# Optimization experiments

Measured on AMD Instinct MI355X. Metric: run time of the kernel, lower is better.

Reference implementation:

```python
import jax, jax.numpy as jnp
import numpy as np

N = 50000      # nodes
E = 800000     # edges (avg degree 16)
IN = 256       # in_feats
H = 128        # hidden_feats
C = 40         # out_feats == num classes (label dim)
LPA_ITERS = 10


def setup_inputs() -> dict:
    key = jax.random.key(0)
    ks = jax.random.split(key, 9)
    features = jax.random.normal(ks[0], (N, IN), dtype=jnp.float32)
    labels = jax.random.normal(ks[1], (N, C), dtype=jnp.float32)
    mask = jax.random.randint(ks[2], (N,), 0, 2) > 0          # bool [N]
    src = jax.random.randint(ks[3], (E,), 0, N, dtype=jnp.int32)
    dst = jax.random.randint(ks[4], (E,), 0, N, dtype=jnp.int32)
    W1 = jax.random.normal(ks[5], (IN, H), dtype=jnp.float32) * (1.0 / np.sqrt(IN))
    b1 = jnp.zeros((H,), dtype=jnp.float32)
    W2 = jax.random.normal(ks[6], (H, C), dtype=jnp.float32) * (1.0 / np.sqrt(H))
    b2 = jnp.zeros((C,), dtype=jnp.float32)
    return {"features": features, "labels": labels, "mask": mask,
            "src": src, "dst": dst, "W1": W1, "b1": b1, "W2": W2, "b2": b2}


def reference(features, labels, mask, src, dst, W1, b1, W2, b2):
    ones_e = jnp.ones((E,), dtype=jnp.float32)
    deg_out = jax.ops.segment_sum(ones_e, src, num_segments=N)  # out-degree
    deg_in = jax.ops.segment_sum(ones_e, dst, num_segments=N)   # in-degree
    norm_src = jnp.maximum(deg_out, 1.0) ** -0.5                 # DGL clamps deg>=1
    norm_dst = jnp.maximum(deg_in, 1.0) ** -0.5

    def gconv(x, W, b):
        # DGL GraphConv, norm='both': D_in^{-1/2} A^T D_out^{-1/2} (x W) + b
        h = (x @ W) * norm_src[:, None]                          # [N, d_out]
        agg = jax.ops.segment_sum(h[src], dst, num_segments=N)   # gather+scatter-add
        return agg * norm_dst[:, None] + b

    x = jax.nn.relu(gconv(features, W1, b1))
    # dropout identity in eval mode
    x = gconv(x, W2, b2)

    # Label propagation: adj[src,dst]=1 so (adj @ y)[i] = sum_{(i->j)} y[j]
    masked_labels = jnp.where(mask[:, None], labels, 0.0)

    def step(y, _):
        y = jax.ops.segment_sum(y[dst], src, num_segments=N)
        y = jnp.where(mask[:, None], labels, y)
        return y, None

    y, _ = jax.lax.scan(step, masked_labels, None, length=LPA_ITERS)
    return x, y
```

## Files before the change

### kernel.cpp

```cpp
#include <hip/hip_runtime.h>

#define Nn 50000
#define Ee 800000
#define INF_ 256
#define HID 128
#define NC 40
#define CAPD 48
#define CAPS 48
#define LPA_ITERS 10
#define NB 98
#define BSH 9
#define EPB 1024
#define NBLK ((Ee + EPB - 1) / EPB)
#define CAPB_D 10240
#define CAPB_S 6144

typedef __attribute__((ext_vector_type(8))) short bfrag;
typedef __attribute__((ext_vector_type(4))) float ffrag;

__device__ inline unsigned f2bf2(float a, float b) {
    unsigned ua = __float_as_uint(a); ua += 0x7FFFu + ((ua >> 16) & 1u);
    unsigned ub = __float_as_uint(b); ub += 0x7FFFu + ((ub >> 16) & 1u);
    return (ua >> 16) | (ub & 0xFFFF0000u);
}
__device__ inline unsigned short f2bf(float a) {
    unsigned ua = __float_as_uint(a); ua += 0x7FFFu + ((ua >> 16) & 1u);
    return (unsigned short)(ua >> 16);
}
__device__ inline float bf_lo(unsigned u) { return __uint_as_float(u << 16); }
__device__ inline float bf_hi(unsigned u) { return __uint_as_float(u & 0xFFFF0000u); }

__global__ void detect_fmt(const unsigned int* __restrict__ m, int* flag) {
    int i = blockIdx.x * blockDim.x + threadIdx.x;
    if (i < 12500) {
        if (m[i] > 1u) atomicOr(flag, 1);
    }
}

__device__ inline bool read_mask(const void* mask, int node, int fmt) {
    if (fmt) return ((const unsigned char*)mask)[node] != 0;
    return ((const int*)mask)[node] != 0;
}

__global__ __launch_bounds__(256) void bin_edges(
    const int* __restrict__ src, const int* __restrict__ dst,
    const void* __restrict__ mask, const int* __restrict__ flag,
    int* __restrict__ cnt_src,
    int* __restrict__ cur_d, int* __restrict__ cur_s,
    unsigned* __restrict__ bkt_d, unsigned* __restrict__ bkt_s) {
    __shared__ unsigned stage_d[EPB];
    __shared__ unsigned stage_s[EPB];
    __shared__ int hd[NB], od[NB + 1], cd[NB], gd_[NB];
    __shared__ int hs[NB], os_[NB + 1], cs_[NB], gs_[NB];
    int tid = threadIdx.x;
    int lane = tid & 63;
    int wid = tid >> 6;
    int e0 = blockIdx.x * EPB;
    int fmt = *flag;
    if (tid < NB) { hd[tid] = 0; hs[tid] = 0; }
    __syncthreads();

    int rs[EPB / 256], rd[EPB / 256];
    unsigned um = 0;
#pragma unroll
    for (int k = 0; k < EPB / 256; k++) {
        int e = e0 + tid + k * 256;
        rs[k] = -1; rd[k] = -1;
        if (e < Ee) {
            int s = src[e], d = dst[e];
            rs[k] = s; rd[k] = d;
            atomicAdd(&cnt_src[s], 1);
            atomicAdd(&hd[d >> BSH], 1);
            if (!read_mask(mask, s, fmt)) {
                um |= (1u << k);
                atomicAdd(&hs[s >> BSH], 1);
            }
        }
    }
    __syncthreads();
    if (wid < 2) {
        int* h = wid ? hs : hd;
        int* o = wid ? os_ : od;
        int i0 = lane * 2;
        int v0 = (i0 < NB) ? h[i0] : 0;
        int v1 = (i0 + 1 < NB) ? h[i0 + 1] : 0;
        int s = v0 + v1;
#pragma unroll
        for (int d = 1; d < 64; d <<= 1) {
            int t = __shfl_up(s, d);
            if (lane >= d) s += t;
        }
        int excl = s - v0 - v1;
        if (i0 < NB) o[i0] = excl;
        if (i0 + 1 < NB) o[i0 + 1] = excl + v0;
        if (lane == 63) o[NB] = s;
    }
    __syncthreads();
    if (tid < NB) {
        gd_[tid] = hd[tid] ? atomicAdd(&cur_d[tid], hd[tid]) : 0;
        gs_[tid] = hs[tid] ? atomicAdd(&cur_s[tid], hs[tid]) : 0;
        cd[tid] = od[tid];
        cs_[tid] = os_[tid];
    }
    __syncthreads();
#pragma unroll
    for (int k = 0; k < EPB / 256; k++) {
        if (rd[k] >= 0) {
            int p = atomicAdd(&cd[rd[k] >> BSH], 1);
            stage_d[p] = ((unsigned)rd[k] << 16) | (unsigned)rs[k];
            if (um & (1u << k)) {
                int q = atomicAdd(&cs_[rs[k] >> BSH], 1);
                stage_s[q] = ((unsigned)rs[k] << 16) | (unsigned)rd[k];
            }
        }
    }
    __syncthreads();
    for (int b = wid; b < NB; b += 4) {
        int base = od[b], cntb = hd[b], g0 = gd_[b];
        unsigned* gb = bkt_d + (size_t)b * CAPB_D;
        for (int i = lane; i < cntb; i += 64) {
            int pos = g0 + i;
            if (pos < CAPB_D) gb[pos] = stage_d[base + i];
        }
        int bs = os_[b], cnts = hs[b], gs0 = gs_[b];
        unsigned* gbs = bkt_s + (size_t)b * CAPB_S;
        for (int i = lane; i < cnts; i += 64) {
            int pos = gs0 + i;
            if (pos < CAPB_S) gbs[pos] = stage_s[bs + i];
        }
    }
}

__global__ __launch_bounds__(256) void build_csr_both(
    const unsigned* __restrict__ bkt_d, const int* __restrict__ cur_d,
    const unsigned* __restrict__ bkt_s, const int* __restrict__ cur_s,
    const void* __restrict__ mask, const int* __restrict__ flag,
    int* __restrict__ adj_dst, int* __restrict__ cnt_dst,
    int* __restrict__ adj_s, int* __restrict__ cnt_u, int* __restrict__ cnt_m,
    int* __restrict__ n_un, int* __restrict__ ulist) {
    __shared__ int lu[512], lm[512];
    int bb = blockIdx.x, tid = threadIdx.x;
    lu[tid] = 0; lu[tid + 256] = 0; lm[tid] = 0; lm[tid + 256] = 0;
    __syncthreads();
    if (bb < NB) {
        int b = bb;
        int n = cur_d[b]; if (n > CAPB_D) n = CAPB_D;
        int n0 = b << BSH;
        const unsigned* base = bkt_d + (size_t)b * CAPB_D;
        for (int i = tid; i < n; i += 256) {
            unsigned r = base[i];
            int d = r >> 16, s = r & 0xffff;
            int sl = atomicAdd(&lu[d - n0], 1);
            if (sl < CAPD) adj_dst[d * CAPD + sl] = s;
        }
        __syncthreads();
        int g0 = n0 + tid;
        if (g0 < Nn) cnt_dst[g0] = lu[tid];
        g0 += 256;
        if (g0 < Nn) cnt_dst[g0] = lu[tid + 256];
    } else {
        int b = bb - NB;
        int fmt = *flag;
        int n = cur_s[b]; if (n > CAPB_S) n = CAPB_S;
        int n0 = b << BSH;
        const unsigned* base = bkt_s + (size_t)b * CAPB_S;
        for (int i = tid; i < n; i += 256) {
            unsigned r = base[i];
            int s = r >> 16, d = r & 0xffff;
            if (read_mask(mask, d, fmt)) {
                int sl = atomicAdd(&lm[s - n0], 1);
                if (sl < CAPS) adj_s[s * CAPS + (CAPS - 1 - sl)] = d;
            } else {
                int sl = atomicAdd(&lu[s - n0], 1);
                if (sl < CAPS) adj_s[s * CAPS + sl] = d;
            }
        }
        __syncthreads();
        int g0 = n0 + tid;
        if (g0 < Nn) {
            cnt_u[g0] = lu[tid]; cnt_m[g0] = lm[tid];
            if (!read_mask(mask, g0, fmt)) {
                int p = atomicAdd(n_un, 1);
                ulist[p] = g0;
            }
        }
        g0 += 256;
        if (g0 < Nn) {
            cnt_u[g0] = lu[tid + 256]; cnt_m[g0] = lm[tid + 256];
            if (!read_mask(mask, g0, fmt)) {
                int p = atomicAdd(n_un, 1);
                ulist[p] = g0;
            }
        }
    }
}

__global__ void prep_w1t(const float* __restrict__ W1,
                         unsigned short* __restrict__ W1t) {
    int c = blockIdx.x;
    int k = threadIdx.x;
    W1t[c * INF_ + k] = f2bf(W1[(size_t)k * HID + c]);
}

#define G1_ROWS 64
__global__ __launch_bounds__(256) void gemm1(
    const float* __restrict__ feat, const unsigned short* __restrict__ W1t,
    const int* __restrict__ cnt_src, unsigned short* __restrict__ h1b) {
    __shared__ unsigned short lA[G1_ROWS * 32];
    __shared__ unsigned short lB[HID * 32];
    const int tid = threadIdx.x;
    const int row0 = blockIdx.x * G1_ROWS;
    const int w = tid >> 6;
    const int l = tid & 63;
    const int lane15 = l & 15;
    const int quad = l >> 4;
    const int rw0 = w * 16;

    ffrag acc[8];
#pragma unroll
    for (int t = 0; t < 8; t++) acc[t] = (ffrag){0.f, 0.f, 0.f, 0.f};

    for (int k0 = 0; k0 < INF_; k0 += 32) {
#pragma unroll
        for (int p = 0; p < 2; p++) {
            int idx = tid + p * 256;
            int r = idx >> 3, c4 = idx & 7;
            int grow = row0 + r;
            float4 v = make_float4(0.f, 0.f, 0.f, 0.f);
            if (grow < Nn)
                v = *(const float4*)(feat + (size_t)grow * INF_ + k0 + c4 * 4);
            uint2 pk;
            pk.x = f2bf2(v.x, v.y);
            pk.y = f2bf2(v.z, v.w);
            *(uint2*)((char*)lA + r * 64 + c4 * 8) = pk;
        }
#pragma unroll
        for (int p = 0; p < 2; p++) {
            int idx = tid + p * 256;
            int col = idx >> 2, q = idx & 3;
            uint4 v = *(const uint4*)((const char*)W1t + col * 512 + k0 * 2 + q * 16);
            *(uint4*)((char*)lB + col * 64 + q * 16) = v;
        }
        __syncthreads();
        int arow = rw0 + lane15;
        bfrag af = *(const bfrag*)((const char*)lA + arow * 64 + quad * 16);
#pragma unroll
        for (int t = 0; t < 8; t++) {
            int col = t * 16 + lane15;
            bfrag bf = *(const bfrag*)((const char*)lB + col * 64 + quad * 16);
            acc[t] = __builtin_amdgcn_mfma_f32_16x16x32_bf16(af, bf, acc[t], 0, 0, 0);
        }
        __syncthreads();
    }
    float nrm[4];
#pragma unroll
    for (int i = 0; i < 4; i++) {
        int grow = row0 + rw0 + quad * 4 + i;
        int dg = (grow < Nn) ? cnt_src[grow] : 1;
        nrm[i] = rsqrtf((float)(dg > 1 ? dg : 1));
    }
#pragma unroll
    for (int t = 0; t < 8; t++) {
#pragma unroll
        for (int i = 0; i < 4; i++) {
            int grow = row0 + rw0 + quad * 4 + i;
            if (grow < Nn)
                h1b[(size_t)grow * HID + t * 16 + lane15] = f2bf(acc[t][i] * nrm[i]);
        }
    }
}

__global__ __launch_bounds__(256) void agg_relu1(
    const uint4* __restrict__ h1b, const int* __restrict__ adj_dst,
    const int* __restrict__ cnt_dst, const float4* __restrict__ b1,
    float4* __restrict__ x1) {
    int node = blockIdx.x * 16 + (threadIdx.x >> 4);
    int l = threadIdx.x & 15;
    int dg = cnt_dst[node];
    int cnt = dg < CAPD ? dg : CAPD;
    const int* lst = adj_dst + (size_t)node * CAPD;
    float s0 = 0.f, s1 = 0.f, s2 = 0.f, s3 = 0.f;
    float s4 = 0.f, s5 = 0.f, s6 = 0.f, s7 = 0.f;
    int e = 0;
    for (; e + 8 <= cnt; e += 8) {
        uint4 u[8];
#pragma unroll
        for (int q = 0; q < 8; q++) u[q] = h1b[(size_t)lst[e + q] * 16 + l];
#pragma unroll
        for (int q = 0; q < 8; q++) {
            s0 += bf_lo(u[q].x); s1 += bf_hi(u[q].x);
            s2 += bf_lo(u[q].y); s3 += bf_hi(u[q].y);
            s4 += bf_lo(u[q].z); s5 += bf_hi(u[q].z);
            s6 += bf_lo(u[q].w); s7 += bf_hi(u[q].w);
        }
    }
    for (; e < cnt; e++) {
        uint4 u = h1b[(size_t)lst[e] * 16 + l];
        s0 += bf_lo(u.x); s1 += bf_hi(u.x);
        s2 += bf_lo(u.y); s3 += bf_hi(u.y);
        s4 += bf_lo(u.z); s5 += bf_hi(u.z);
        s6 += bf_lo(u.w); s7 += bf_hi(u.w);
    }
    float nrm = rsqrtf((float)(dg > 1 ? dg : 1));
    float4 bb0 = b1[l * 2], bb1 = b1[l * 2 + 1];
    float4 v0, v1;
    v0.x = fmaxf(s0 * nrm + bb0.x, 0.f);
    v0.y = fmaxf(s1 * nrm + bb0.y, 0.f);
    v0.z = fmaxf(s2 * nrm + bb0.z, 0.f);
    v0.w = fmaxf(s3 * nrm + bb0.w, 0.f);
    v1.x = fmaxf(s4 * nrm + bb1.x, 0.f);
    v1.y = fmaxf(s5 * nrm + bb1.y, 0.f);
    v1.z = fmaxf(s6 * nrm + bb1.z, 0.f);
    v1.w = fmaxf(s7 * nrm + bb1.w, 0.f);
    x1[(size_t)node * 32 + l * 2] = v0;
    x1[(size_t)node * 32 + l * 2 + 1] = v1;
}

__global__ __launch_bounds__(256) void gemm2(
    const float4* __restrict__ x1, const float4* __restrict__ W2,
    const int* __restrict__ cnt_src, unsigned* __restrict__ h2b) {
    __shared__ float lw[HID * NC];
    int tid = threadIdx.x;
    for (int i = tid; i < HID * NC / 4; i += 256)
        ((float4*)lw)[i] = W2[i];
    __syncthreads();
    int r = blockIdx.x * 256 + tid;
    if (r >= Nn) return;
    const float4* xr = x1 + (size_t)r * 32;
    float4 acc[10];
#pragma unroll
    for (int j = 0; j < 10; j++) acc[j] = make_float4(0.f, 0.f, 0.f, 0.f);
    for (int k4 = 0; k4 < 32; k4++) {
        float4 xv = xr[k4];
#pragma unroll
        for (int s = 0; s < 4; s++) {
            float x = s == 0 ? xv.x : (s == 1 ? xv.y : (s == 2 ? xv.z : xv.w));
            const float4* wrow = (const float4*)(lw + (k4 * 4 + s) * NC);
#pragma unroll
            for (int j = 0; j < 10; j++) {
                float4 w = wrow[j];
                acc[j].x += x * w.x; acc[j].y += x * w.y;
                acc[j].z += x * w.z; acc[j].w += x * w.w;
            }
        }
    }
    int dg = cnt_src[r];
    float nrm = rsqrtf((float)(dg > 1 ? dg : 1));
    uint2* out = (uint2*)(h2b + (size_t)r * 20);
#pragma unroll
    for (int j = 0; j < 10; j++) {
        uint2 pk;
        pk.x = f2bf2(acc[j].x * nrm, acc[j].y * nrm);
        pk.y = f2bf2(acc[j].z * nrm, acc[j].w * nrm);
        out[j] = pk;
    }
}

__global__ __launch_bounds__(320) void agg2(
    const uint2* __restrict__ h2b, const int* __restrict__ adj_dst,
    const int* __restrict__ cnt_dst, const float4* __restrict__ b2,
    float4* __restrict__ out_x) {
    int node = blockIdx.x * 32 + threadIdx.x / 10;
    int l = threadIdx.x % 10;
    if (node >= Nn) return;
    int dg = cnt_dst[node];
    int cnt = dg < CAPD ? dg : CAPD;
    const int* lst = adj_dst + (size_t)node * CAPD;
    float s0 = 0.f, s1 = 0.f, s2 = 0.f, s3 = 0.f;
    int e = 0;
    for (; e + 8 <= cnt; e += 8) {
        uint2 u[8];
#pragma unroll
        for (int q = 0; q < 8; q++) u[q] = h2b[(size_t)lst[e + q] * 10 + l];
#pragma unroll
        for (int q = 0; q < 8; q++) {
            s0 += bf_lo(u[q].x); s1 += bf_hi(u[q].x);
            s2 += bf_lo(u[q].y); s3 += bf_hi(u[q].y);
        }
    }
    for (; e + 4 <= cnt; e += 4) {
        uint2 u[4];
#pragma unroll
        for (int q = 0; q < 4; q++) u[q] = h2b[(size_t)lst[e + q] * 10 + l];
#pragma unroll
        for (int q = 0; q < 4; q++) {
            s0 += bf_lo(u[q].x); s1 += bf_hi(u[q].x);
            s2 += bf_lo(u[q].y); s3 += bf_hi(u[q].y);
        }
    }
    for (; e < cnt; e++) {
        uint2 u = h2b[(size_t)lst[e] * 10 + l];
        s0 += bf_lo(u.x); s1 += bf_hi(u.x);
        s2 += bf_lo(u.y); s3 += bf_hi(u.y);
    }
    float nrm = rsqrtf((float)(dg > 1 ? dg : 1));
    float4 bb = b2[l];
    float4 v;
    v.x = s0 * nrm + bb.x;
    v.y = s1 * nrm + bb.y;
    v.z = s2 * nrm + bb.z;
    v.w = s3 * nrm + bb.w;
    out_x[(size_t)node * 10 + l] = v;
}

__global__ void lpa_init(const float* __restrict__ labels, const void* mask,
                         const int* __restrict__ flag, float* __restrict__ out_y) {
    int g = blockIdx.x * blockDim.x + threadIdx.x;
    if (g >= Nn * NC) return;
    int node = g / NC;
    if (read_mask(mask, node, *flag)) out_y[g] = labels[g];
}

__global__ __launch_bounds__(320) void lpa_const(
    const float4* __restrict__ labels, const int* __restrict__ n_un,
    const int* __restrict__ ulist, const int* __restrict__ adj_s,
    const int* __restrict__ cnt_m, float4* __restrict__ sconst,
    uint2* __restrict__ y1b) {
    int g = blockIdx.x * 32 + threadIdx.x / 10;
    int l = threadIdx.x % 10;
    if (g >= *n_un) return;
    int u = ulist[g];
    int cm = cnt_m[u];
    int cnt = cm < CAPS ? cm : CAPS;
    const int* lst = adj_s + (size_t)u * CAPS + (CAPS - cnt);
    float4 s = make_float4(0.f, 0.f, 0.f, 0.f);
    int e = 0;
    for (; e + 8 <= cnt; e += 8) {
        float4 v[8];
#pragma unroll
        for (int q = 0; q < 8; q++) v[q] = labels[(size_t)lst[e + q] * 10 + l];
#pragma unroll
        for (int q = 0; q < 8; q++) {
            s.x += v[q].x; s.y += v[q].y; s.z += v[q].z; s.w += v[q].w;
        }
    }
    for (; e + 4 <= cnt; e += 4) {
        float4 v[4];
#pragma unroll
        for (int q = 0; q < 4; q++) v[q] = labels[(size_t)lst[e + q] * 10 + l];
#pragma unroll
        for (int q = 0; q < 4; q++) {
            s.x += v[q].x; s.y += v[q].y; s.z += v[q].z; s.w += v[q].w;
        }
    }
    for (; e < cnt; e++) {
        float4 a = labels[(size_t)lst[e] * 10 + l];
        s.x += a.x; s.y += a.y; s.z += a.z; s.w += a.w;
    }
    sconst[(size_t)u * 10 + l] = s;
    uint2 pk; pk.x = f2bf2(s.x, s.y); pk.y = f2bf2(s.z, s.w);
    y1b[(size_t)u * 10 + l] = pk;
}

__global__ __launch_bounds__(320) void lpa_mid(
    const uint2* __restrict__ ycur, const int* __restrict__ n_un,
    const int* __restrict__ ulist, const int* __restrict__ adj_s,
    const int* __restrict__ cnt_u, const float4* __restrict__ sconst,
    uint2* __restrict__ ynext) {
    int g = blockIdx.x * 32 + threadIdx.x / 10;
    int l = threadIdx.x % 10;
    if (g >= *n_un) return;
    int u = ulist[g];
    int cu = cnt_u[u];
    int cnt = cu < CAPS ? cu : CAPS;
    const int* lst = adj_s + (size_t)u * CAPS;
    float4 s = sconst[(size_t)u * 10 + l];
    int e = 0;
    for (; e + 8 <= cnt; e += 8) {
        uint2 v[8];
#pragma unroll
        for (int q = 0; q < 8; q++) v[q] = ycur[(size_t)lst[e + q] * 10 + l];
#pragma unroll
        for (int q = 0; q < 8; q++) {
            s.x += bf_lo(v[q].x); s.y += bf_hi(v[q].x);
            s.z += bf_lo(v[q].y); s.w += bf_hi(v[q].y);
        }
    }
    for (; e + 4 <= cnt; e += 4) {
        uint2 v[4];
#pragma unroll
        for (int q = 0; q < 4; q++) v[q] = ycur[(size_t)lst[e + q] * 10 + l];
#pragma unroll
        for (int q = 0; q < 4; q++) {
            s.x += bf_lo(v[q].x); s.y += bf_hi(v[q].x);
            s.z += bf_lo(v[q].y); s.w += bf_hi(v[q].y);
        }
    }
    for (; e < cnt; e++) {
        uint2 v = ycur[(size_t)lst[e] * 10 + l];
        s.x += bf_lo(v.x); s.y += bf_hi(v.x);
        s.z += bf_lo(v.y); s.w += bf_hi(v.y);
    }
    uint2 pk; pk.x = f2bf2(s.x, s.y); pk.y = f2bf2(s.z, s.w);
    ynext[(size_t)u * 10 + l] = pk;
}

__global__ __launch_bounds__(320) void lpa_last(
    const uint2* __restrict__ ycur, const int* __restrict__ n_un,
    const int* __restrict__ ulist, const int* __restrict__ adj_s,
    const int* __restrict__ cnt_u, const float4* __restrict__ sconst,
    float4* __restrict__ out_y) {
    int g = blockIdx.x * 32 + threadIdx.x / 10;
    int l = threadIdx.x % 10;
    if (g >= *n_un) return;
    int u = ulist[g];
    int cu = cnt_u[u];
    int cnt = cu < CAPS ? cu : CAPS;
    const int* lst = adj_s + (size_t)u * CAPS;
    float4 s = sconst[(size_t)u * 10 + l];
    int e = 0;
    for (; e + 8 <= cnt; e += 8) {
        uint2 v[8];
#pragma unroll
        for (int q = 0; q < 8; q++) v[q] = ycur[(size_t)lst[e + q] * 10 + l];
#pragma unroll
        for (int q = 0; q < 8; q++) {
            s.x += bf_lo(v[q].x); s.y += bf_hi(v[q].x);
            s.z += bf_lo(v[q].y); s.w += bf_hi(v[q].y);
        }
    }
    for (; e + 4 <= cnt; e += 4) {
        uint2 v[4];
#pragma unroll
        for (int q = 0; q < 4; q++) v[q] = ycur[(size_t)lst[e + q] * 10 + l];
#pragma unroll
        for (int q = 0; q < 4; q++) {
            s.x += bf_lo(v[q].x); s.y += bf_hi(v[q].x);
            s.z += bf_lo(v[q].y); s.w += bf_hi(v[q].y);
        }
    }
    for (; e < cnt; e++) {
        uint2 v = ycur[(size_t)lst[e] * 10 + l];
        s.x += bf_lo(v.x); s.y += bf_hi(v.x);
        s.z += bf_lo(v.y); s.w += bf_hi(v.y);
    }
    out_y[(size_t)u * 10 + l] = s;
}

extern "C" void kernel_launch(void* const* d_in, const int* in_sizes, int n_in,
                              void* d_out, int out_size, void* d_ws, size_t ws_size,
                              hipStream_t stream) {
    const float* feat   = (const float*)d_in[0];
    const float* labels = (const float*)d_in[1];
    const void*  mask   = d_in[2];
    const int*   src    = (const int*)d_in[3];
    const int*   dst    = (const int*)d_in[4];
    const float* W1     = (const float*)d_in[5];
    const float* b1     = (const float*)d_in[6];
    const float* W2     = (const float*)d_in[7];
    const float* b2     = (const float*)d_in[8];

    float* out_x = (float*)d_out;
    float* out_y = out_x + (size_t)Nn * NC;

    char* ws = (char*)d_ws;
    size_t off = 0;
    auto alloc = [&](size_t bytes) -> void* {
        void* p = ws + off;
        off += (bytes + 255) & ~(size_t)255;
        return p;
    };
    int* flag    = (int*)alloc(256);
    int* n_un    = flag + 1;
    int* cnt_src = (int*)alloc((size_t)Nn * 4);
    int* cur_d   = (int*)alloc(512);
    int* cur_s   = (int*)alloc(512);
    size_t zero_bytes = off;
    int* cnt_dst = (int*)alloc((size_t)Nn * 4);
    int* cnt_u   = (int*)alloc((size_t)Nn * 4);
    int* cnt_m   = (int*)alloc((size_t)Nn * 4);
    int* ulist   = (int*)alloc((size_t)Nn * 4);
    unsigned short* W1t = (unsigned short*)alloc((size_t)HID * INF_ * 2);
    char* uni = (char*)alloc((size_t)Nn * HID * 2);
    unsigned* bkt_d = (unsigned*)uni;
    unsigned* bkt_s = (unsigned*)(uni + (size_t)NB * CAPB_D * 4);
    unsigned short* h1b = (unsigned short*)uni;
    float* x1 = (float*)alloc((size_t)Nn * HID * 4);
    int* adj_s   = (int*)alloc((size_t)Nn * CAPS * 4);
    int* adj_dst = (int*)alloc((size_t)Nn * CAPD * 4);
    unsigned* h2b = (unsigned*)alloc((size_t)Nn * NC * 2);
    float* sconst = (float*)alloc((size_t)Nn * NC * 4);
    uint2* y1b = (uint2*)alloc((size_t)Nn * NC * 2);
    uint2* y2b = (uint2*)alloc((size_t)Nn * NC * 2);

    hipMemsetAsync(d_ws, 0, zero_bytes, stream);

    detect_fmt<<<49, 256, 0, stream>>>((const unsigned int*)mask, flag);
    prep_w1t<<<HID, INF_, 0, stream>>>(W1, W1t);
    bin_edges<<<NBLK, 256, 0, stream>>>(src, dst, mask, flag, cnt_src,
                                        cur_d, cur_s, bkt_d, bkt_s);
    build_csr_both<<<NB * 2, 256, 0, stream>>>(bkt_d, cur_d, bkt_s, cur_s,
                                               mask, flag, adj_dst, cnt_dst,
                                               adj_s, cnt_u, cnt_m, n_un, ulist);

    gemm1<<<(Nn + G1_ROWS - 1) / G1_ROWS, 256, 0, stream>>>(feat, W1t, cnt_src, h1b);
    agg_relu1<<<Nn / 16, 256, 0, stream>>>((const uint4*)h1b, adj_dst, cnt_dst,
                                           (const float4*)b1, (float4*)x1);
    gemm2<<<196, 256, 0, stream>>>((const float4*)x1, (const float4*)W2,
                                   cnt_src, h2b);
    agg2<<<(Nn + 31) / 32, 320, 0, stream>>>((const uint2*)h2b, adj_dst, cnt_dst,
                                             (const float4*)b2, (float4*)out_x);

    lpa_init<<<(Nn * NC + 255) / 256, 256, 0, stream>>>(labels, mask, flag, out_y);
    lpa_const<<<(Nn + 31) / 32, 320, 0, stream>>>(
        (const float4*)labels, n_un, ulist, adj_s, cnt_m, (float4*)sconst, y1b);
    const uint2* cur = y1b;
    for (int i = 0; i < 8; i++) {
        uint2* nxt = (i & 1) ? y1b : y2b;
        lpa_mid<<<(Nn + 31) / 32, 320, 0, stream>>>(
            cur, n_un, ulist, adj_s, cnt_u, (const float4*)sconst, nxt);
        cur = nxt;
    }
    lpa_last<<<(Nn + 31) / 32, 320, 0, stream>>>(
        cur, n_un, ulist, adj_s, cnt_u, (const float4*)sconst, (float4*)out_y);
}
```

Baseline: 393.0 us.

## Fuse edge binning with first GEMM and fold LPA init into lpa_const

Edge binning and the first feature GEMM now run in one launch, with block ranges split by blockIdx, so the bandwidth-heavy GEMM can overlap the atomic-heavy binning. To remove the GEMM's dependency on out-degree counts, the source normalisation is moved out of the GEMM epilogue: build_csr_both computes a per-node nrm_s array, and agg_relu1 gathers and multiplies it per edge. The masked-label copy that lpa_init did is folded into lpa_const, which drops one more launch. In exchange, h1b and the bucket buffers no longer share memory, and the first aggregation does an extra scalar gather and multiply per edge.

```diff
diff --git a/kernel.cpp b/kernel.cpp
--- a/kernel.cpp
+++ b/kernel.cpp
@@ -12,6 +12,8 @@
 #define BSH 9
 #define EPB 1024
 #define NBLK ((Ee + EPB - 1) / EPB)
+#define G1_ROWS 64
+#define G1BLK ((Nn + G1_ROWS - 1) / G1_ROWS)
 #define CAPB_D 10240
 #define CAPB_S 6144
 
@@ -42,91 +44,163 @@
     return ((const int*)mask)[node] != 0;
 }
 
-__global__ __launch_bounds__(256) void bin_edges(
+__global__ void prep_w1t(const float* __restrict__ W1,
+                         unsigned short* __restrict__ W1t) {
+    int c = blockIdx.x;
+    int k = threadIdx.x;
+    W1t[c * INF_ + k] = f2bf(W1[(size_t)k * HID + c]);
+}
+
+__global__ __launch_bounds__(256) void phase1(
     const int* __restrict__ src, const int* __restrict__ dst,
     const void* __restrict__ mask, const int* __restrict__ flag,
-    int* __restrict__ cnt_src,
-    int* __restrict__ cur_d, int* __restrict__ cur_s,
-    unsigned* __restrict__ bkt_d, unsigned* __restrict__ bkt_s) {
-    __shared__ unsigned stage_d[EPB];
-    __shared__ unsigned stage_s[EPB];
-    __shared__ int hd[NB], od[NB + 1], cd[NB], gd_[NB];
-    __shared__ int hs[NB], os_[NB + 1], cs_[NB], gs_[NB];
-    int tid = threadIdx.x;
-    int lane = tid & 63;
-    int wid = tid >> 6;
-    int e0 = blockIdx.x * EPB;
-    int fmt = *flag;
-    if (tid < NB) { hd[tid] = 0; hs[tid] = 0; }
-    __syncthreads();
-
-    int rs[EPB / 256], rd[EPB / 256];
-    unsigned um = 0;
-#pragma unroll
-    for (int k = 0; k < EPB / 256; k++) {
-        int e = e0 + tid + k * 256;
-        rs[k] = -1; rd[k] = -1;
-        if (e < Ee) {
-            int s = src[e], d = dst[e];
-            rs[k] = s; rd[k] = d;
-            atomicAdd(&cnt_src[s], 1);
-            atomicAdd(&hd[d >> BSH], 1);
-            if (!read_mask(mask, s, fmt)) {
-                um |= (1u << k);
-                atomicAdd(&hs[s >> BSH], 1);
-            }
-        }
-    }
-    __syncthreads();
-    if (wid < 2) {
-        int* h = wid ? hs : hd;
-        int* o = wid ? os_ : od;
-        int i0 = lane * 2;
-        int v0 = (i0 < NB) ? h[i0] : 0;
-        int v1 = (i0 + 1 < NB) ? h[i0 + 1] : 0;
-        int s = v0 + v1;
-#pragma unroll
-        for (int d = 1; d < 64; d <<= 1) {
-            int t = __shfl_up(s, d);
-            if (lane >= d) s += t;
-        }
-        int excl = s - v0 - v1;
-        if (i0 < NB) o[i0] = excl;
-        if (i0 + 1 < NB) o[i0 + 1] = excl + v0;
-        if (lane == 63) o[NB] = s;
-    }
-    __syncthreads();
-    if (tid < NB) {
-        gd_[tid] = hd[tid] ? atomicAdd(&cur_d[tid], hd[tid]) : 0;
-        gs_[tid] = hs[tid] ? atomicAdd(&cur_s[tid], hs[tid]) : 0;
-        cd[tid] = od[tid];
-        cs_[tid] = os_[tid];
-    }
-    __syncthreads();
-#pragma unroll
-    for (int k = 0; k < EPB / 256; k++) {
-        if (rd[k] >= 0) {
-            int p = atomicAdd(&cd[rd[k] >> BSH], 1);
-            stage_d[p] = ((unsigned)rd[k] << 16) | (unsigned)rs[k];
-            if (um & (1u << k)) {
-                int q = atomicAdd(&cs_[rs[k] >> BSH], 1);
-                stage_s[q] = ((unsigned)rs[k] << 16) | (unsigned)rd[k];
-            }
-        }
-    }
-    __syncthreads();
-    for (int b = wid; b < NB; b += 4) {
-        int base = od[b], cntb = hd[b], g0 = gd_[b];
-        unsigned* gb = bkt_d + (size_t)b * CAPB_D;
-        for (int i = lane; i < cntb; i += 64) {
-            int pos = g0 + i;
-            if (pos < CAPB_D) gb[pos] = stage_d[base + i];
-        }
-        int bs = os_[b], cnts = hs[b], gs0 = gs_[b];
-        unsigned* gbs = bkt_s + (size_t)b * CAPB_S;
-        for (int i = lane; i < cnts; i += 64) {
-            int pos = gs0 + i;
-            if (pos < CAPB_S) gbs[pos] = stage_s[bs + i];
+    int* __restrict__ cnt_src, int* __restrict__ cur_d, int* __restrict__ cur_s,
+    unsigned* __restrict__ bkt_d, unsigned* __restrict__ bkt_s,
+    const float* __restrict__ feat, const unsigned short* __restrict__ W1t,
+    unsigned short* __restrict__ h1b) {
+    __shared__ uint4 smem[784];
+    const int tid = threadIdx.x;
+    if (blockIdx.x < NBLK) {
+        unsigned* stage_d = (unsigned*)smem;
+        unsigned* stage_s = stage_d + EPB;
+        int* hd  = (int*)(stage_s + EPB);
+        int* od  = hd + NB;
+        int* cd  = od + NB + 1;
+        int* gd_ = cd + NB;
+        int* hs  = gd_ + NB;
+        int* os_ = hs + NB;
+        int* cs_ = os_ + NB + 1;
+        int* gs_ = cs_ + NB;
+        int lane = tid & 63;
+        int wid = tid >> 6;
+        int e0 = blockIdx.x * EPB;
+        int fmt = *flag;
+        if (tid < NB) { hd[tid] = 0; hs[tid] = 0; }
+        __syncthreads();
+
+        int rs[EPB / 256], rd[EPB / 256];
+        unsigned um = 0;
+#pragma unroll
+        for (int k = 0; k < EPB / 256; k++) {
+            int e = e0 + tid + k * 256;
+            rs[k] = -1; rd[k] = -1;
+            if (e < Ee) {
+                int s = src[e], d = dst[e];
+                rs[k] = s; rd[k] = d;
+                atomicAdd(&cnt_src[s], 1);
+                atomicAdd(&hd[d >> BSH], 1);
+                if (!read_mask(mask, s, fmt)) {
+                    um |= (1u << k);
+                    atomicAdd(&hs[s >> BSH], 1);
+                }
+            }
+        }
+        __syncthreads();
+        if (wid < 2) {
+            int* h = wid ? hs : hd;
+            int* o = wid ? os_ : od;
+            int i0 = lane * 2;
+            int v0 = (i0 < NB) ? h[i0] : 0;
+            int v1 = (i0 + 1 < NB) ? h[i0 + 1] : 0;
+            int s = v0 + v1;
+#pragma unroll
+            for (int d = 1; d < 64; d <<= 1) {
+                int t = __shfl_up(s, d);
+                if (lane >= d) s += t;
+            }
+            int excl = s - v0 - v1;
+            if (i0 < NB) o[i0] = excl;
+            if (i0 + 1 < NB) o[i0 + 1] = excl + v0;
+            if (lane == 63) o[NB] = s;
+        }
+        __syncthreads();
+        if (tid < NB) {
+            gd_[tid] = hd[tid] ? atomicAdd(&cur_d[tid], hd[tid]) : 0;
+            gs_[tid] = hs[tid] ? atomicAdd(&cur_s[tid], hs[tid]) : 0;
+            cd[tid] = od[tid];
+            cs_[tid] = os_[tid];
+        }
+        __syncthreads();
+#pragma unroll
+        for (int k = 0; k < EPB / 256; k++) {
+            if (rd[k] >= 0) {
+                int p = atomicAdd(&cd[rd[k] >> BSH], 1);
+                stage_d[p] = ((unsigned)rd[k] << 16) | (unsigned)rs[k];
+                if (um & (1u << k)) {
+                    int q = atomicAdd(&cs_[rs[k] >> BSH], 1);
+                    stage_s[q] = ((unsigned)rs[k] << 16) | (unsigned)rd[k];
+                }
+            }
+        }
+        __syncthreads();
+        for (int b = wid; b < NB; b += 4) {
+            int base = od[b], cntb = hd[b], g0 = gd_[b];
+            unsigned* gb = bkt_d + (size_t)b * CAPB_D;
+            for (int i = lane; i < cntb; i += 64) {
+                int pos = g0 + i;
+                if (pos < CAPB_D) gb[pos] = stage_d[base + i];
+            }
+            int bs = os_[b], cnts = hs[b], gs0 = gs_[b];
+            unsigned* gbs = bkt_s + (size_t)b * CAPB_S;
+            for (int i = lane; i < cnts; i += 64) {
+                int pos = gs0 + i;
+                if (pos < CAPB_S) gbs[pos] = stage_s[bs + i];
+            }
+        }
+    } else {
+        unsigned short* lA = (unsigned short*)smem;
+        unsigned short* lB = lA + G1_ROWS * 32;
+        const int row0 = (blockIdx.x - NBLK) * G1_ROWS;
+        const int w = tid >> 6;
+        const int l = tid & 63;
+        const int lane15 = l & 15;
+        const int quad = l >> 4;
+        const int rw0 = w * 16;
+
+        ffrag acc[8];
+#pragma unroll
+        for (int t = 0; t < 8; t++) acc[t] = (ffrag){0.f, 0.f, 0.f, 0.f};
+
+        for (int k0 = 0; k0 < INF_; k0 += 32) {
+#pragma unroll
+            for (int p = 0; p < 2; p++) {
+                int idx = tid + p * 256;
+                int r = idx >> 3, c4 = idx & 7;
+                int grow = row0 + r;
+                float4 v = make_float4(0.f, 0.f, 0.f, 0.f);
+                if (grow < Nn)
+                    v = *(const float4*)(feat + (size_t)grow * INF_ + k0 + c4 * 4);
+                uint2 pk;
+                pk.x = f2bf2(v.x, v.y);
+                pk.y = f2bf2(v.z, v.w);
+                *(uint2*)((char*)lA + r * 64 + c4 * 8) = pk;
+            }
+#pragma unroll
+            for (int p = 0; p < 2; p++) {
+                int idx = tid + p * 256;
+                int col = idx >> 2, q = idx & 3;
+                uint4 v = *(const uint4*)((const char*)W1t + col * 512 + k0 * 2 + q * 16);
+                *(uint4*)((char*)lB + col * 64 + q * 16) = v;
+            }
+            __syncthreads();
+            int arow = rw0 + lane15;
+            bfrag af = *(const bfrag*)((const char*)lA + arow * 64 + quad * 16);
+#pragma unroll
+            for (int t = 0; t < 8; t++) {
+                int col = t * 16 + lane15;
+                bfrag bf = *(const bfrag*)((const char*)lB + col * 64 + quad * 16);
+                acc[t] = __builtin_amdgcn_mfma_f32_16x16x32_bf16(af, bf, acc[t], 0, 0, 0);
+            }
+            __syncthreads();
+        }
+#pragma unroll
+        for (int t = 0; t < 8; t++) {
+#pragma unroll
+            for (int i = 0; i < 4; i++) {
+                int grow = row0 + rw0 + quad * 4 + i;
+                if (grow < Nn)
+                    h1b[(size_t)grow * HID + t * 16 + lane15] = f2bf(acc[t][i]);
+            }
         }
     }
 }
@@ -135,9 +209,10 @@
     const unsigned* __restrict__ bkt_d, const int* __restrict__ cur_d,
     const unsigned* __restrict__ bkt_s, const int* __restrict__ cur_s,
     const void* __restrict__ mask, const int* __restrict__ flag,
+    const int* __restrict__ cnt_src,
     int* __restrict__ adj_dst, int* __restrict__ cnt_dst,
     int* __restrict__ adj_s, int* __restrict__ cnt_u, int* __restrict__ cnt_m,
-    int* __restrict__ n_un, int* __restrict__ ulist) {
+    float* __restrict__ nrm_s, int* __restrict__ n_un, int* __restrict__ ulist) {
     __shared__ int lu[512], lm[512];
     int bb = blockIdx.x, tid = threadIdx.x;
     lu[tid] = 0; lu[tid + 256] = 0; lm[tid] = 0; lm[tid + 256] = 0;
@@ -179,6 +254,8 @@
         int g0 = n0 + tid;
         if (g0 < Nn) {
             cnt_u[g0] = lu[tid]; cnt_m[g0] = lm[tid];
+            int cs = cnt_src[g0];
+            nrm_s[g0] = rsqrtf((float)(cs > 1 ? cs : 1));
             if (!read_mask(mask, g0, fmt)) {
                 int p = atomicAdd(n_un, 1);
                 ulist[p] = g0;
@@ -187,6 +264,8 @@
         g0 += 256;
         if (g0 < Nn) {
             cnt_u[g0] = lu[tid + 256]; cnt_m[g0] = lm[tid + 256];
+            int cs = cnt_src[g0];
+            nrm_s[g0] = rsqrtf((float)(cs > 1 ? cs : 1));
             if (!read_mask(mask, g0, fmt)) {
                 int p = atomicAdd(n_un, 1);
                 ulist[p] = g0;
@@ -195,85 +274,10 @@
     }
 }
 
-__global__ void prep_w1t(const float* __restrict__ W1,
-                         unsigned short* __restrict__ W1t) {
-    int c = blockIdx.x;
-    int k = threadIdx.x;
-    W1t[c * INF_ + k] = f2bf(W1[(size_t)k * HID + c]);
-}
-
-#define G1_ROWS 64
-__global__ __launch_bounds__(256) void gemm1(
-    const float* __restrict__ feat, const unsigned short* __restrict__ W1t,
-    const int* __restrict__ cnt_src, unsigned short* __restrict__ h1b) {
-    __shared__ unsigned short lA[G1_ROWS * 32];
-    __shared__ unsigned short lB[HID * 32];
-    const int tid = threadIdx.x;
-    const int row0 = blockIdx.x * G1_ROWS;
-    const int w = tid >> 6;
-    const int l = tid & 63;
-    const int lane15 = l & 15;
-    const int quad = l >> 4;
-    const int rw0 = w * 16;
-
-    ffrag acc[8];
-#pragma unroll
-    for (int t = 0; t < 8; t++) acc[t] = (ffrag){0.f, 0.f, 0.f, 0.f};
-
-    for (int k0 = 0; k0 < INF_; k0 += 32) {
-#pragma unroll
-        for (int p = 0; p < 2; p++) {
-            int idx = tid + p * 256;
-            int r = idx >> 3, c4 = idx & 7;
-            int grow = row0 + r;
-            float4 v = make_float4(0.f, 0.f, 0.f, 0.f);
-            if (grow < Nn)
-                v = *(const float4*)(feat + (size_t)grow * INF_ + k0 + c4 * 4);
-            uint2 pk;
-            pk.x = f2bf2(v.x, v.y);
-            pk.y = f2bf2(v.z, v.w);
-            *(uint2*)((char*)lA + r * 64 + c4 * 8) = pk;
-        }
-#pragma unroll
-        for (int p = 0; p < 2; p++) {
-            int idx = tid + p * 256;
-            int col = idx >> 2, q = idx & 3;
-            uint4 v = *(const uint4*)((const char*)W1t + col * 512 + k0 * 2 + q * 16);
-            *(uint4*)((char*)lB + col * 64 + q * 16) = v;
-        }
-        __syncthreads();
-        int arow = rw0 + lane15;
-        bfrag af = *(const bfrag*)((const char*)lA + arow * 64 + quad * 16);
-#pragma unroll
-        for (int t = 0; t < 8; t++) {
-            int col = t * 16 + lane15;
-            bfrag bf = *(const bfrag*)((const char*)lB + col * 64 + quad * 16);
-            acc[t] = __builtin_amdgcn_mfma_f32_16x16x32_bf16(af, bf, acc[t], 0, 0, 0);
-        }
-        __syncthreads();
-    }
-    float nrm[4];
-#pragma unroll
-    for (int i = 0; i < 4; i++) {
-        int grow = row0 + rw0 + quad * 4 + i;
-        int dg = (grow < Nn) ? cnt_src[grow] : 1;
-        nrm[i] = rsqrtf((float)(dg > 1 ? dg : 1));
-    }
-#pragma unroll
-    for (int t = 0; t < 8; t++) {
-#pragma unroll
-        for (int i = 0; i < 4; i++) {
-            int grow = row0 + rw0 + quad * 4 + i;
-            if (grow < Nn)
-                h1b[(size_t)grow * HID + t * 16 + lane15] = f2bf(acc[t][i] * nrm[i]);
-        }
-    }
-}
-
 __global__ __launch_bounds__(256) void agg_relu1(
     const uint4* __restrict__ h1b, const int* __restrict__ adj_dst,
-    const int* __restrict__ cnt_dst, const float4* __restrict__ b1,
-    float4* __restrict__ x1) {
+    const int* __restrict__ cnt_dst, const float* __restrict__ nrm_s,
+    const float4* __restrict__ b1, float4* __restrict__ x1) {
     int node = blockIdx.x * 16 + (threadIdx.x >> 4);
     int l = threadIdx.x & 15;
     int dg = cnt_dst[node];
@@ -283,23 +287,29 @@
     float s4 = 0.f, s5 = 0.f, s6 = 0.f, s7 = 0.f;
     int e = 0;
     for (; e + 8 <= cnt; e += 8) {
-        uint4 u[8];
-#pragma unroll
-        for (int q = 0; q < 8; q++) u[q] = h1b[(size_t)lst[e + q] * 16 + l];
+        uint4 u[8]; float ns[8];
 #pragma unroll
         for (int q = 0; q < 8; q++) {
-            s0 += bf_lo(u[q].x); s1 += bf_hi(u[q].x);
-            s2 += bf_lo(u[q].y); s3 += bf_hi(u[q].y);
-            s4 += bf_lo(u[q].z); s5 += bf_hi(u[q].z);
-            s6 += bf_lo(u[q].w); s7 += bf_hi(u[q].w);
+            int sidx = lst[e + q];
+            u[q] = h1b[(size_t)sidx * 16 + l];
+            ns[q] = nrm_s[sidx];
+        }
+#pragma unroll
+        for (int q = 0; q < 8; q++) {
+            s0 += ns[q] * bf_lo(u[q].x); s1 += ns[q] * bf_hi(u[q].x);
+            s2 += ns[q] * bf_lo(u[q].y); s3 += ns[q] * bf_hi(u[q].y);
+            s4 += ns[q] * bf_lo(u[q].z); s5 += ns[q] * bf_hi(u[q].z);
+            s6 += ns[q] * bf_lo(u[q].w); s7 += ns[q] * bf_hi(u[q].w);
         }
     }
     for (; e < cnt; e++) {
-        uint4 u = h1b[(size_t)lst[e] * 16 + l];
-        s0 += bf_lo(u.x); s1 += bf_hi(u.x);
-        s2 += bf_lo(u.y); s3 += bf_hi(u.y);
-        s4 += bf_lo(u.z); s5 += bf_hi(u.z);
-        s6 += bf_lo(u.w); s7 += bf_hi(u.w);
+        int sidx = lst[e];
+        uint4 u = h1b[(size_t)sidx * 16 + l];
+        float nsv = nrm_s[sidx];
+        s0 += nsv * bf_lo(u.x); s1 += nsv * bf_hi(u.x);
+        s2 += nsv * bf_lo(u.y); s3 += nsv * bf_hi(u.y);
+        s4 += nsv * bf_lo(u.z); s5 += nsv * bf_hi(u.z);
+        s6 += nsv * bf_lo(u.w); s7 += nsv * bf_hi(u.w);
     }
     float nrm = rsqrtf((float)(dg > 1 ? dg : 1));
     float4 bb0 = b1[l * 2], bb1 = b1[l * 2 + 1];
@@ -403,19 +413,18 @@
     out_x[(size_t)node * 10 + l] = v;
 }
 
-__global__ void lpa_init(const float* __restrict__ labels, const void* mask,
-                         const int* __restrict__ flag, float* __restrict__ out_y) {
-    int g = blockIdx.x * blockDim.x + threadIdx.x;
-    if (g >= Nn * NC) return;
-    int node = g / NC;
-    if (read_mask(mask, node, *flag)) out_y[g] = labels[g];
-}
-
 __global__ __launch_bounds__(320) void lpa_const(
-    const float4* __restrict__ labels, const int* __restrict__ n_un,
+    const float4* __restrict__ labels, const void* __restrict__ mask,
+    const int* __restrict__ flag, const int* __restrict__ n_un,
     const int* __restrict__ ulist, const int* __restrict__ adj_s,
     const int* __restrict__ cnt_m, float4* __restrict__ sconst,
-    uint2* __restrict__ y1b) {
+    uint2* __restrict__ y1b, float4* __restrict__ out_y4) {
+    int fmt = *flag;
+    int i = blockIdx.x * 320 + threadIdx.x;
+    if (i < Nn * 10) {
+        int node = i / 10;
+        if (read_mask(mask, node, fmt)) out_y4[i] = labels[i];
+    }
     int g = blockIdx.x * 32 + threadIdx.x / 10;
     int l = threadIdx.x % 10;
     if (g >= *n_un) return;
@@ -570,11 +579,11 @@
     int* cnt_u   = (int*)alloc((size_t)Nn * 4);
     int* cnt_m   = (int*)alloc((size_t)Nn * 4);
     int* ulist   = (int*)alloc((size_t)Nn * 4);
+    float* nrm_s = (float*)alloc((size_t)Nn * 4);
     unsigned short* W1t = (unsigned short*)alloc((size_t)HID * INF_ * 2);
-    char* uni = (char*)alloc((size_t)Nn * HID * 2);
-    unsigned* bkt_d = (unsigned*)uni;
-    unsigned* bkt_s = (unsigned*)(uni + (size_t)NB * CAPB_D * 4);
-    unsigned short* h1b = (unsigned short*)uni;
+    unsigned* bkt_d = (unsigned*)alloc((size_t)NB * CAPB_D * 4);
+    unsigned* bkt_s = (unsigned*)alloc((size_t)NB * CAPB_S * 4);
+    unsigned short* h1b = (unsigned short*)alloc((size_t)Nn * HID * 2);
     float* x1 = (float*)alloc((size_t)Nn * HID * 4);
     int* adj_s   = (int*)alloc((size_t)Nn * CAPS * 4);
     int* adj_dst = (int*)alloc((size_t)Nn * CAPD * 4);
@@ -587,23 +596,23 @@
 
     detect_fmt<<<49, 256, 0, stream>>>((const unsigned int*)mask, flag);
     prep_w1t<<<HID, INF_, 0, stream>>>(W1, W1t);
-    bin_edges<<<NBLK, 256, 0, stream>>>(src, dst, mask, flag, cnt_src,
-                                        cur_d, cur_s, bkt_d, bkt_s);
-    build_csr_both<<<NB * 2, 256, 0, stream>>>(bkt_d, cur_d, bkt_s, cur_s,
-                                               mask, flag, adj_dst, cnt_dst,
-                                               adj_s, cnt_u, cnt_m, n_un, ulist);
-
-    gemm1<<<(Nn + G1_ROWS - 1) / G1_ROWS, 256, 0, stream>>>(feat, W1t, cnt_src, h1b);
+    phase1<<<NBLK + G1BLK, 256, 0, stream>>>(
+        src, dst, mask, flag, cnt_src, cur_d, cur_s, bkt_d, bkt_s,
+        feat, W1t, h1b);
+    build_csr_both<<<NB * 2, 256, 0, stream>>>(
+        bkt_d, cur_d, bkt_s, cur_s, mask, flag, cnt_src,
+        adj_dst, cnt_dst, adj_s, cnt_u, cnt_m, nrm_s, n_un, ulist);
+
     agg_relu1<<<Nn / 16, 256, 0, stream>>>((const uint4*)h1b, adj_dst, cnt_dst,
-                                           (const float4*)b1, (float4*)x1);
+                                           nrm_s, (const float4*)b1, (float4*)x1);
     gemm2<<<196, 256, 0, stream>>>((const float4*)x1, (const float4*)W2,
                                    cnt_src, h2b);
     agg2<<<(Nn + 31) / 32, 320, 0, stream>>>((const uint2*)h2b, adj_dst, cnt_dst,
                                              (const float4*)b2, (float4*)out_x);
 
-    lpa_init<<<(Nn * NC + 255) / 256, 256, 0, stream>>>(labels, mask, flag, out_y);
     lpa_const<<<(Nn + 31) / 32, 320, 0, stream>>>(
-        (const float4*)labels, n_un, ulist, adj_s, cnt_m, (float4*)sconst, y1b);
+        (const float4*)labels, mask, flag, n_un, ulist, adj_s, cnt_m,
+        (float4*)sconst, y1b, (float4*)out_y);
     const uint2* cur = y1b;
     for (int i = 0; i < 8; i++) {
         uint2* nxt = (i & 1) ? y1b : y2b;
```

Result: faster. 380.4 us (-3.2%).
